# Optimization experiments

Hardware: AMD Instinct MI355X
Metric: run time of the kernel (lower is better)

Reference implementation:

```python
import jax, jax.numpy as jnp
import numpy as np

N, D, C, K, M = 32768, 512, 64, 16, 512
DEPTH = 4          # log2(K)
NODES = K - 1      # 15 internal nodes per codebook


def _create_selection_matrix(C, K):
    # maps the DEPTH features of each codebook to its 15 internal-node comparisons
    S = np.zeros((C * NODES, C * DEPTH), dtype=np.float32)
    for c in range(C):
        for i in range(NODES):
            level = 0 if i == 0 else (1 if i < 3 else (2 if i < 7 else 3))
            S[c * NODES + i, c * DEPTH + level] = 1.0
    return S


def _create_bit_matrix(C, K):
    # leaf-vs-path sign matrix of a balanced depth-4 tree, block-diagonal over C
    Bm = np.zeros((C * K, C * NODES), dtype=np.float32)
    for c in range(C):
        for k in range(K):
            node = 0
            for level in range(DEPTH):
                bit = (k >> (DEPTH - 1 - level)) & 1
                Bm[c * K + k, c * NODES + node] = 1.0 if bit else -1.0
                node = 2 * node + 1 + bit
    return Bm


def setup_inputs() -> dict:
    key = jax.random.key(0)
    k_i, k_t, k_l, k_a = jax.random.split(key, 4)
    I = jax.random.normal(k_i, (N, D), dtype=jnp.float32)
    T = jax.random.uniform(k_t, (C * NODES,), dtype=jnp.float32)           # thresholds, U[0,1)
    fan_l = C * K
    L = jax.random.uniform(k_l, (M, C, K), dtype=jnp.float32,
                           minval=-1.0, maxval=1.0) * np.sqrt(3.0 / fan_l)  # kaiming-uniform-ish
    A = jax.random.uniform(k_a, (D, C * DEPTH), dtype=jnp.float32,
                           minval=-1.0, maxval=1.0) * np.sqrt(3.0 / D)
    S = jnp.asarray(_create_selection_matrix(C, K))
    B = jnp.asarray(_create_bit_matrix(C, K))
    return {"I": I, "T": T, "L": L, "A": A, "S": S, "B": B}


def reference(I, T, L, A, S, B):
    Mm, Cc, Kk = L.shape
    P = I @ A                                    # (N, C*DEPTH) learned projection
    h = P @ S.T - T[None, :]                     # (N, 15C) node comparisons
    t = jnp.tanh(h)
    # straight-through hard sign for the tree decisions
    h_st = t + jax.lax.stop_gradient(jnp.sign(h) - t)
    b = (h_st @ B.T).reshape(-1, Cc, Kk)         # (N, C, K) leaf scores
    soft = jax.nn.softmax(b, axis=-1)
    hard = jax.nn.one_hot(jnp.argmax(b, axis=-1), Kk, dtype=I.dtype)
    E = soft + jax.lax.stop_gradient(hard - soft)  # straight-through one-hot encoding
    # per-subspace LUT gather + sum over codebooks
    return jnp.einsum("nck,mck->nm", E, L)       # (N, M)
```

## Files before the change

kernel.cpp:

```cpp
#include <hip/hip_runtime.h>
#include <stdint.h>


#define DDIM 512
#define CD4 256
#define CKDIM 1024
#define MOUT 512
#define NODES 15
#define CAP (1u << 20)

typedef unsigned short u16;
typedef unsigned int u32;
typedef __attribute__((ext_vector_type(8))) __bf16 bf16x8;
typedef __attribute__((ext_vector_type(4))) float f32x4;
typedef __attribute__((ext_vector_type(4))) u32 u32x4;
typedef __attribute__((ext_vector_type(2))) u32 u32x2;

__device__ __forceinline__ void gld_lds16(const void* g, void* l) {
  __builtin_amdgcn_global_load_lds(
      (const __attribute__((address_space(1))) void*)g,
      (__attribute__((address_space(3))) void*)l, 16, 0, 0);
}
__device__ __forceinline__ float bf2f(u16 u) {
  uint32_t x = ((uint32_t)u) << 16; return __builtin_bit_cast(float, x);
}
__device__ __forceinline__ u16 f2bf(float f) {
  uint32_t x = __builtin_bit_cast(uint32_t, f);
  return (u16)((x + 0x7FFFu + ((x >> 16) & 1u)) >> 16);
}

__global__ __launch_bounds__(256) void k0_prep(const float* __restrict__ Ag,
                                               u16* __restrict__ Ath,
                                               u16* __restrict__ Atl,
                                               const float* __restrict__ Lg,
                                               u16* __restrict__ Lb,
                                               u32* __restrict__ flagcnt) {
  const int bx = blockIdx.x, t = threadIdx.x;
  if (bx < 32) {
    __shared__ float Tl[64][65];
    const int cx = bx & 3, ky = bx >> 2;
    const int lane = t & 63, w = t >> 6;
#pragma unroll
    for (int rr = 0; rr < 16; ++rr) {
      int r = w * 16 + rr;
      Tl[r][lane] = Ag[(size_t)(ky * 64 + r) * CD4 + cx * 64 + lane];
    }
    __syncthreads();
#pragma unroll
    for (int rr = 0; rr < 16; ++rr) {
      int c = w * 16 + rr;
      float x = Tl[lane][c];
      u16 h = f2bf(x);
      u16 l = f2bf(x - bf2f(h));
      size_t o = (size_t)(cx * 64 + c) * DDIM + ky * 64 + lane;
      Ath[o] = h;
      Atl[o] = l;
    }
  } else {
    if (bx == 32 && t == 0) *flagcnt = 0;
    int i = ((bx - 32) * 256 + t) * 4;
    f32x4 v = *(const f32x4*)(Lg + i);
    u32 lo = (u32)f2bf(v[0]) | ((u32)f2bf(v[1]) << 16);
    u32 hi = (u32)f2bf(v[2]) | ((u32)f2bf(v[3]) << 16);
    *(u32*)(Lb + i) = lo;
    *(u32*)(Lb + i + 2) = hi;
  }
}

__global__ __launch_bounds__(256, 4) void k1_p_codes(
    const float* __restrict__ Ig, const u16* __restrict__ Ath,
    const float* __restrict__ Tg,
    uint8_t* __restrict__ codes, u32* __restrict__ flagcnt,
    u32* __restrict__ flaglist) {
  __shared__ __align__(16) char smem[36864];
  float* If = (float*)smem;
  u16* Bt = (u16*)(smem + 4096);

  const int t = threadIdx.x, nb = blockIdx.x;
  const int lane = t & 63, wave = t >> 6, quad = lane >> 4, l16 = lane & 15;

  f32x4 acc[2][4] = {};

  for (int kb = 0; kb < 16; ++kb) {
    __syncthreads();
    {
      int r = t >> 3, s = t & 7, g = s ^ (r & 7);
      gld_lds16(Ig + (size_t)(nb * 32 + r) * DDIM + kb * 32 + g * 4, If + t * 4);
    }
#pragma unroll
    for (int q = 0; q < 8; ++q) {
      int cid = t + q * 256, r = cid >> 3, s = cid & 7, g = s ^ (r & 7);
      gld_lds16(Ath + (size_t)(g >> 2) * (256 * DDIM) +
                    (size_t)r * DDIM + kb * 32 + (g & 3) * 8,
                Bt + cid * 8);
    }
    __syncthreads();

    bf16x8 ah[2], al[2], bh[4], bl[4];
#pragma unroll
    for (int i = 0; i < 2; ++i) {
      int ra = i * 16 + l16;
      int s0 = ra * 8 + ((quad * 2) ^ (ra & 7));
      int s1 = ra * 8 + ((quad * 2 + 1) ^ (ra & 7));
      f32x4 c0 = *(const f32x4*)(If + s0 * 4);
      f32x4 c1 = *(const f32x4*)(If + s1 * 4);
      float xs[8] = {c0[0], c0[1], c0[2], c0[3], c1[0], c1[1], c1[2], c1[3]};
      u32 hw[4], lw[4];
#pragma unroll
      for (int p = 0; p < 4; ++p) {
        u32 u0 = __builtin_bit_cast(u32, xs[2 * p]);
        u32 u1 = __builtin_bit_cast(u32, xs[2 * p + 1]);
        hw[p] = __builtin_amdgcn_perm(u1, u0, 0x07060302);
        float h0 = __builtin_bit_cast(float, u0 & 0xFFFF0000u);
        float h1 = __builtin_bit_cast(float, u1 & 0xFFFF0000u);
        u32 l0 = __builtin_bit_cast(u32, xs[2 * p] - h0);
        u32 l1 = __builtin_bit_cast(u32, xs[2 * p + 1] - h1);
        lw[p] = __builtin_amdgcn_perm(l1, l0, 0x07060302);
      }
      ah[i] = __builtin_bit_cast(bf16x8, (u32x4){hw[0], hw[1], hw[2], hw[3]});
      al[i] = __builtin_bit_cast(bf16x8, (u32x4){lw[0], lw[1], lw[2], lw[3]});
    }
#pragma unroll
    for (int j = 0; j < 4; ++j) {
      int rb = wave * 64 + j * 16 + l16;
      int sh = quad ^ (rb & 7), sl = (4 + quad) ^ (rb & 7);
      bh[j] = *(const bf16x8*)(Bt + (rb * 8 + sh) * 8);
      bl[j] = *(const bf16x8*)(Bt + (rb * 8 + sl) * 8);
    }
    __builtin_amdgcn_s_setprio(1);
#pragma unroll
    for (int i = 0; i < 2; ++i)
#pragma unroll
      for (int j = 0; j < 4; ++j) {
        acc[i][j] = __builtin_amdgcn_mfma_f32_16x16x32_bf16(ah[i], bh[j], acc[i][j], 0, 0, 0);
        acc[i][j] = __builtin_amdgcn_mfma_f32_16x16x32_bf16(ah[i], bl[j], acc[i][j], 0, 0, 0);
        acc[i][j] = __builtin_amdgcn_mfma_f32_16x16x32_bf16(al[i], bh[j], acc[i][j], 0, 0, 0);
      }
    __builtin_amdgcn_s_setprio(0);
  }

  __syncthreads();
  float* Tl = (float*)smem;
  uint8_t* codes_lds = (uint8_t*)(smem + 4096);
  u32* flagbuf = (u32*)(smem + 8192);
  u32* fmeta = (u32*)(smem + 16384);
  if (t < 240) *(f32x4*)(Tl + t * 4) = *(const f32x4*)(Tg + t * 4);
  __syncthreads();

  u32 wcnt = 0;
#pragma unroll
  for (int i = 0; i < 2; ++i)
#pragma unroll
    for (int j = 0; j < 4; ++j) {
      f32x4 v = acc[i][j];
      {
        float x = (l16 & 1) ? v[0] : v[1];
        float y = (l16 & 1) ? v[2] : v[3];
        x = __shfl_xor(x, 1);
        y = __shfl_xor(y, 1);
        if (l16 & 1) { v[0] = x; v[2] = y; } else { v[1] = x; v[3] = y; }
        float p = (l16 & 2) ? v[0] : v[2];
        float q = (l16 & 2) ? v[1] : v[3];
        p = __shfl_xor(p, 2);
        q = __shfl_xor(q, 2);
        if (l16 & 2) { v[0] = p; v[1] = q; } else { v[2] = p; v[3] = q; }
      }
      int row = i * 16 + quad * 4 + (l16 & 3);
      int cg = wave * 16 + j * 4 + (l16 >> 2);
      const float* Tc = Tl + cg * NODES;
      int node = 0, k = 0;
      float mm = 1e30f;
#pragma unroll
      for (int l = 0; l < 4; ++l) {
        float h = v[l] - Tc[node];
        mm = fminf(mm, __builtin_fabsf(h));
        int bit = h > 0.0f ? 1 : 0;
        k = (k << 1) | bit;
        node = 2 * node + 1 + bit;
      }
      codes_lds[row * 64 + cg] = (uint8_t)k;
      bool fl = mm < 2e-3f;
      unsigned long long bm = __ballot(fl);
      if (bm) {
        if (fl) {
          int rank = __popcll(bm & ((1ull << lane) - 1ull));
          flagbuf[wave * 512 + wcnt + rank] =
              ((u32)(nb * 32 + row) << 6) | (u32)cg;
        }
        wcnt += (u32)__popcll(bm);
      }
    }
  if (lane == 0) fmeta[wave] = wcnt;
  __syncthreads();
  {
    u32 c0 = fmeta[0], c1 = fmeta[1], c2 = fmeta[2], c3 = fmeta[3];
    u32 total = c0 + c1 + c2 + c3;
    if (t == 0 && total) fmeta[4] = atomicAdd(flagcnt, total);
    *(u32x2*)(codes + (size_t)nb * 2048 + t * 8) =
        *(const u32x2*)(codes_lds + t * 8);
    __syncthreads();
    if (total) {
      u32 base = fmeta[4];
      u32 pre = (wave > 0 ? c0 : 0) + (wave > 1 ? c1 : 0) + (wave > 2 ? c2 : 0);
      u32 mycnt = fmeta[wave];
      for (u32 i2 = (u32)lane; i2 < mycnt; i2 += 64) {
        u32 pos = base + pre + i2;
        if (pos < CAP) flaglist[pos] = flagbuf[wave * 512 + i2];
      }
    }
  }
}

__global__ __launch_bounds__(256) void k1b_rescue(
    const float* __restrict__ Ig, const float* __restrict__ Ag,
    const float* __restrict__ Tg, const u32* __restrict__ cnt,
    const u32* __restrict__ list, uint8_t* __restrict__ codes) {
  u32 total = *cnt;
  if (total > CAP) total = CAP;
  const int lane = threadIdx.x & 63;
  const u32 wid = (u32)((blockIdx.x * blockDim.x + threadIdx.x) >> 6);
  const u32 nw = (u32)((gridDim.x * blockDim.x) >> 6);
  for (u32 e = wid; e < total; e += nw) {
    u32 v = list[e];
    int n = v >> 6, c = v & 63;
    const float* Ir = Ig + (size_t)n * DDIM;
    const float* Ac = Ag + c * 4;
    double p0 = 0.0, p1 = 0.0, p2 = 0.0, p3 = 0.0;
#pragma unroll
    for (int u = 0; u < 8; ++u) {
      int d = u * 64 + lane;
      double iv = (double)Ir[d];
      f32x4 a = *(const f32x4*)(Ac + (size_t)d * CD4);
      p0 += iv * (double)a[0]; p1 += iv * (double)a[1];
      p2 += iv * (double)a[2]; p3 += iv * (double)a[3];
    }
#pragma unroll
    for (int off = 32; off; off >>= 1) {
      p0 += __shfl_xor(p0, off);
      p1 += __shfl_xor(p1, off);
      p2 += __shfl_xor(p2, off);
      p3 += __shfl_xor(p3, off);
    }
    if (lane == 0) {
      double p[4] = {p0, p1, p2, p3};
      const float* Tc = Tg + c * NODES;
      int node = 0, k = 0;
      for (int l = 0; l < 4; ++l) {
        int bit = p[l] > (double)Tc[node] ? 1 : 0;
        k = (k << 1) | bit;
        node = 2 * node + 1 + bit;
      }
      codes[(size_t)n * 64 + c] = (uint8_t)k;
    }
  }
}

__global__ __launch_bounds__(256, 3) void k2_out(
    const uint8_t* __restrict__ codes, const u16* __restrict__ Lb,
    float* __restrict__ Og) {
  __shared__ __align__(16) u16 Ltile[128 * 64];
  __shared__ __align__(16) uint8_t codesT[64 * 128];
  __shared__ __align__(16) u16 lut[32 * 8];

  const int t = threadIdx.x, mb = blockIdx.x, nb = blockIdx.y;
  const int lane = t & 63, wave = t >> 6, quad = lane >> 4, l16 = lane & 15;
  const int wr = wave >> 1, wc = wave & 1;

  if (t < 32) {
    int h = t >> 4, v = t & 15;
#pragma unroll
    for (int j = 0; j < 8; ++j)
      lut[t * 8 + j] = (v == h * 8 + j) ? (u16)0x3F80 : (u16)0;
  }
  {
    int n = t >> 1, part = t & 1;
    const u32* src = (const u32*)(codes + (size_t)(nb * 128 + n) * 64 + part * 32);
#pragma unroll
    for (int i = 0; i < 8; ++i) {
      u32 w = src[i];
      int c4 = part * 32 + i * 4;
      codesT[(c4 + 0) * 128 + n] = (uint8_t)(w & 0xff);
      codesT[(c4 + 1) * 128 + n] = (uint8_t)((w >> 8) & 0xff);
      codesT[(c4 + 2) * 128 + n] = (uint8_t)((w >> 16) & 0xff);
      codesT[(c4 + 3) * 128 + n] = (uint8_t)((w >> 24) & 0xff);
    }
  }

  f32x4 acc[4][4] = {};

  for (int kb = 0; kb < 16; ++kb) {
    __syncthreads();
#pragma unroll
    for (int q = 0; q < 4; ++q) {
      int cid = t + q * 256, r = cid >> 3, s = cid & 7, g = s ^ (r & 7);
      gld_lds16(Lb + (size_t)(mb * 128 + r) * CKDIM + kb * 64 + g * 8,
                Ltile + cid * 8);
    }
    __syncthreads();

#pragma unroll
    for (int ks = 0; ks < 2; ++ks) {
      const int c0 = kb * 4 + ks * 2 + (quad >> 1);
      const int h = quad & 1;
      bf16x8 a[4], b[4];
#pragma unroll
      for (int i = 0; i < 4; ++i) {
        int row = wr * 64 + i * 16 + l16;
        int v = codesT[c0 * 128 + row] & 15;
        a[i] = *(const bf16x8*)(lut + (h * 16 + v) * 8);
      }
#pragma unroll
      for (int j = 0; j < 4; ++j) {
        int rm = wc * 64 + j * 16 + l16;
        int slot = (ks * 4 + quad) ^ (rm & 7);
        b[j] = *(const bf16x8*)(Ltile + rm * 64 + slot * 8);
      }
      __builtin_amdgcn_s_setprio(1);
#pragma unroll
      for (int i = 0; i < 4; ++i)
#pragma unroll
        for (int j = 0; j < 4; ++j)
          acc[i][j] = __builtin_amdgcn_mfma_f32_16x16x32_bf16(a[i], b[j], acc[i][j], 0, 0, 0);
      __builtin_amdgcn_s_setprio(0);
    }
  }

#pragma unroll
  for (int i = 0; i < 4; ++i)
#pragma unroll
    for (int j = 0; j < 4; ++j) {
      int row = nb * 128 + wr * 64 + i * 16 + quad * 4;
      int col = mb * 128 + wc * 64 + j * 16 + l16;
#pragma unroll
      for (int r = 0; r < 4; ++r)
        Og[(size_t)(row + r) * MOUT + col] = acc[i][j][r];
    }
}

extern "C" void kernel_launch(void* const* d_in, const int* in_sizes, int n_in,
                              void* d_out, int out_size, void* d_ws, size_t ws_size,
                              hipStream_t stream) {
  const float* Ig = (const float*)d_in[0];
  const float* Tg = (const float*)d_in[1];
  const float* Lg = (const float*)d_in[2];
  const float* Ag = (const float*)d_in[3];
  float* Og = (float*)d_out;

  char* ws = (char*)d_ws;
  u32* cnt = (u32*)ws;
  u32* list = (u32*)(ws + 4096);
  uint8_t* codes = (uint8_t*)(ws + (8u << 20));
  u16* Ath = (u16*)(ws + (10u << 20));
  u16* Atl = Ath + 256 * DDIM;
  u16* Lbf = (u16*)(ws + (10u << 20) + (512u << 10));

  k0_prep<<<dim3(544), dim3(256), 0, stream>>>(Ag, Ath, Atl, Lg, Lbf, cnt);
  k1_p_codes<<<dim3(1024), dim3(256), 0, stream>>>(Ig, Ath, Tg, codes, cnt, list);
  k1b_rescue<<<dim3(512), dim3(256), 0, stream>>>(Ig, Ag, Tg, cnt, list, codes);
  k2_out<<<dim3(4, 256), dim3(256), 0, stream>>>(codes, Lbf, Og);
}
```

Before: 213.4 us.

## Fuse near-threshold rescue into code kernel, dropping global flag list and atomics

Near-threshold (row, codebook) entries are now recomputed in fp64 inside the code-generation kernel. Each wave walks its own LDS flag buffer and patches the codes in LDS before the block writes them out. This removes the separate rescue kernel launch, the global atomic counter, the flag-list round trip and the counter reset in prep. In exchange, rescue work is serialized per wave inside the main kernel, so blocks with many flagged entries take longer, and there is no cross-block load balancing.

```diff
diff --git a/kernel.cpp b/kernel.cpp
--- a/kernel.cpp
+++ b/kernel.cpp
@@ -7,7 +7,6 @@
 #define CKDIM 1024
 #define MOUT 512
 #define NODES 15
-#define CAP (1u << 20)
 
 typedef unsigned short u16;
 typedef unsigned int u32;
@@ -33,8 +32,7 @@
                                                u16* __restrict__ Ath,
                                                u16* __restrict__ Atl,
                                                const float* __restrict__ Lg,
-                                               u16* __restrict__ Lb,
-                                               u32* __restrict__ flagcnt) {
+                                               u16* __restrict__ Lb) {
   const int bx = blockIdx.x, t = threadIdx.x;
   if (bx < 32) {
     __shared__ float Tl[64][65];
@@ -57,7 +55,6 @@
       Atl[o] = l;
     }
   } else {
-    if (bx == 32 && t == 0) *flagcnt = 0;
     int i = ((bx - 32) * 256 + t) * 4;
     f32x4 v = *(const f32x4*)(Lg + i);
     u32 lo = (u32)f2bf(v[0]) | ((u32)f2bf(v[1]) << 16);
@@ -69,9 +66,8 @@
 
 __global__ __launch_bounds__(256, 4) void k1_p_codes(
     const float* __restrict__ Ig, const u16* __restrict__ Ath,
-    const float* __restrict__ Tg,
-    uint8_t* __restrict__ codes, u32* __restrict__ flagcnt,
-    u32* __restrict__ flaglist) {
+    const float* __restrict__ Tg, const float* __restrict__ Ag,
+    uint8_t* __restrict__ codes) {
   __shared__ __align__(16) char smem[36864];
   float* If = (float*)smem;
   u16* Bt = (u16*)(smem + 4096);
@@ -143,7 +139,6 @@
   float* Tl = (float*)smem;
   uint8_t* codes_lds = (uint8_t*)(smem + 4096);
   u32* flagbuf = (u32*)(smem + 8192);
-  u32* fmeta = (u32*)(smem + 16384);
   if (t < 240) *(f32x4*)(Tl + t * 4) = *(const f32x4*)(Tg + t * 4);
   __syncthreads();
 
@@ -184,47 +179,17 @@
       if (bm) {
         if (fl) {
           int rank = __popcll(bm & ((1ull << lane) - 1ull));
-          flagbuf[wave * 512 + wcnt + rank] =
-              ((u32)(nb * 32 + row) << 6) | (u32)cg;
+          flagbuf[wave * 512 + wcnt + rank] = ((u32)row << 6) | (u32)cg;
         }
         wcnt += (u32)__popcll(bm);
       }
     }
-  if (lane == 0) fmeta[wave] = wcnt;
-  __syncthreads();
-  {
-    u32 c0 = fmeta[0], c1 = fmeta[1], c2 = fmeta[2], c3 = fmeta[3];
-    u32 total = c0 + c1 + c2 + c3;
-    if (t == 0 && total) fmeta[4] = atomicAdd(flagcnt, total);
-    *(u32x2*)(codes + (size_t)nb * 2048 + t * 8) =
-        *(const u32x2*)(codes_lds + t * 8);
-    __syncthreads();
-    if (total) {
-      u32 base = fmeta[4];
-      u32 pre = (wave > 0 ? c0 : 0) + (wave > 1 ? c1 : 0) + (wave > 2 ? c2 : 0);
-      u32 mycnt = fmeta[wave];
-      for (u32 i2 = (u32)lane; i2 < mycnt; i2 += 64) {
-        u32 pos = base + pre + i2;
-        if (pos < CAP) flaglist[pos] = flagbuf[wave * 512 + i2];
-      }
-    }
-  }
-}
-
-__global__ __launch_bounds__(256) void k1b_rescue(
-    const float* __restrict__ Ig, const float* __restrict__ Ag,
-    const float* __restrict__ Tg, const u32* __restrict__ cnt,
-    const u32* __restrict__ list, uint8_t* __restrict__ codes) {
-  u32 total = *cnt;
-  if (total > CAP) total = CAP;
-  const int lane = threadIdx.x & 63;
-  const u32 wid = (u32)((blockIdx.x * blockDim.x + threadIdx.x) >> 6);
-  const u32 nw = (u32)((gridDim.x * blockDim.x) >> 6);
-  for (u32 e = wid; e < total; e += nw) {
-    u32 v = list[e];
-    int n = v >> 6, c = v & 63;
-    const float* Ir = Ig + (size_t)n * DDIM;
-    const float* Ac = Ag + c * 4;
+
+  for (u32 e = 0; e < wcnt; ++e) {
+    u32 v = flagbuf[wave * 512 + e];
+    int row = (int)(v >> 6), cg = (int)(v & 63);
+    const float* Ir = Ig + (size_t)(nb * 32 + row) * DDIM;
+    const float* Ac = Ag + cg * 4;
     double p0 = 0.0, p1 = 0.0, p2 = 0.0, p3 = 0.0;
 #pragma unroll
     for (int u = 0; u < 8; ++u) {
@@ -243,16 +208,19 @@
     }
     if (lane == 0) {
       double p[4] = {p0, p1, p2, p3};
-      const float* Tc = Tg + c * NODES;
+      const float* Tc = Tl + cg * NODES;
       int node = 0, k = 0;
       for (int l = 0; l < 4; ++l) {
         int bit = p[l] > (double)Tc[node] ? 1 : 0;
         k = (k << 1) | bit;
         node = 2 * node + 1 + bit;
       }
-      codes[(size_t)n * 64 + c] = (uint8_t)k;
-    }
-  }
+      codes_lds[row * 64 + cg] = (uint8_t)k;
+    }
+  }
+  __syncthreads();
+  *(u32x2*)(codes + (size_t)nb * 2048 + t * 8) =
+      *(const u32x2*)(codes_lds + t * 8);
 }
 
 __global__ __launch_bounds__(256, 3) void k2_out(
@@ -347,15 +315,12 @@
   float* Og = (float*)d_out;
 
   char* ws = (char*)d_ws;
-  u32* cnt = (u32*)ws;
-  u32* list = (u32*)(ws + 4096);
   uint8_t* codes = (uint8_t*)(ws + (8u << 20));
   u16* Ath = (u16*)(ws + (10u << 20));
   u16* Atl = Ath + 256 * DDIM;
   u16* Lbf = (u16*)(ws + (10u << 20) + (512u << 10));
 
-  k0_prep<<<dim3(544), dim3(256), 0, stream>>>(Ag, Ath, Atl, Lg, Lbf, cnt);
-  k1_p_codes<<<dim3(1024), dim3(256), 0, stream>>>(Ig, Ath, Tg, codes, cnt, list);
-  k1b_rescue<<<dim3(512), dim3(256), 0, stream>>>(Ig, Ag, Tg, cnt, list, codes);
+  k0_prep<<<dim3(544), dim3(256), 0, stream>>>(Ag, Ath, Atl, Lg, Lbf);
+  k1_p_codes<<<dim3(1024), dim3(256), 0, stream>>>(Ig, Ath, Tg, Ag, codes);
   k2_out<<<dim3(4, 256), dim3(256), 0, stream>>>(codes, Lbf, Og);
 }
```

Result: no change. 214.0 us (+0.3%).
